# Kernel optimization log

Hardware: AMD Instinct MI355X
Metric: run time of the kernel (lower is better)

Reference implementation:

```python
import jax, jax.numpy as jnp
import numpy as np

V, E, H, G, L, T, B = 32000, 1024, 16, 4, 8, 1024, 2
NKV = H // G          # kv heads = 4
D = E // H            # head dim = 64
BLOCK = 1024          # block_size
EPS = 1e-5


def setup_inputs() -> dict:
    key = jax.random.key(0)
    ks = jax.random.split(key, 12)
    f32 = jnp.float32
    return {
        "idx": jax.random.randint(ks[0], (B, T), 0, V),
        "tok_emb": jax.random.normal(ks[1], (V, E), f32),
        "pos_emb": jax.random.normal(ks[2], (BLOCK, E), f32),
        "q_proj": jax.random.normal(ks[3], (L, E, G, NKV, D), f32) / E**0.5,
        "kv_proj": jax.random.normal(ks[4], (L, 2, E, NKV, D), f32) / E**0.5,
        "out_proj": jax.random.normal(ks[5], (L, E, E), f32) / (D * H)**0.5,
        "fc_in": jax.random.normal(ks[6], (L, E, 4 * E), f32) / E**0.5,
        "fc_out": jax.random.normal(ks[7], (L, 4 * E, E), f32) / (4 * E)**0.5,
        "scale": jnp.ones((L, 2, E), f32),
        "out_scale": jnp.ones((E,), f32),
        "lm_head": jax.random.normal(ks[8], (E, V), f32) / E**0.5,
    }


def _ln(x, w):
    mu = jnp.mean(x, axis=-1, keepdims=True)
    var = jnp.var(x, axis=-1, keepdims=True)
    return (x - mu) * jax.lax.rsqrt(var + EPS) * w


def reference(idx, tok_emb, pos_emb, q_proj, kv_proj, out_proj, fc_in, fc_out, scale, out_scale, lm_head):
    x = tok_emb[idx] + pos_emb[:T]                         # [B,T,E]
    causal = jnp.tril(jnp.ones((T, T), bool))              # [T,T]
    neg_inf = jnp.float32(-jnp.inf)

    def layer(x, params):
        w_kv, w_q, w_out, fc1, fc2, lscale = params
        h = _ln(x, lscale[0])                              # pre-LN (note: residual uses h, matching source)
        q = jnp.einsum('btc,cgnd->bgntd', h, w_q)          # [B,G,NKV,T,D]
        kv = jnp.einsum('btc,scnd->sbntd', h, w_kv)        # [2,B,NKV,T,D]
        k, v = kv[0], kv[1]
        att = jnp.einsum('bgnqd,bnkd->bgnqk', q, k) * (D ** -0.5)
        att = jnp.where(causal, att, neg_inf)
        att = jax.nn.softmax(att, axis=-1)
        o = jnp.einsum('bgnqk,bnkd->bgnqd', att, v)        # [B,G,NKV,T,D]
        o = jnp.transpose(o, (0, 3, 1, 2, 4)).reshape(B, T, E)
        o = jnp.einsum('btc,cd->btd', o, w_out)
        h = h + o
        h = _ln(h, lscale[1])
        mlp = jax.nn.relu(jnp.einsum('btc,cf->btf', h, fc1))
        mlp = jnp.einsum('btf,fc->btc', mlp, fc2)
        return h + mlp, None

    x, _ = jax.lax.scan(layer, x, (kv_proj, q_proj, out_proj, fc_in, fc_out, scale))
    x = _ln(x, out_scale)
    logits = jnp.einsum('btc,cv->btv', x, lm_head)         # [B,T,V]
    return logits
```

## Files before the change

kernel.cpp:

```cpp
#include <hip/hip_runtime.h>
#include <hip/hip_bf16.h>

typedef __attribute__((ext_vector_type(8))) short bf16x8;
typedef __attribute__((ext_vector_type(4))) short bf16x4;
typedef __attribute__((ext_vector_type(4))) float f32x4;

#define LB __launch_bounds__(256)

__device__ __forceinline__ unsigned short f2b(float f) {
  __hip_bfloat16 h = __float2bfloat16(f);
  return __builtin_bit_cast(unsigned short, h);
}

#define GLDS(gp, lp)                                                        \
  __builtin_amdgcn_global_load_lds(                                         \
      (const __attribute__((address_space(1))) void*)(gp),                  \
      (__attribute__((address_space(3))) void*)(lp), 16, 0, 0)

__global__ LB void embed_kernel(const int* __restrict__ idx, const float* __restrict__ tok,
                                const float* __restrict__ pos, float* __restrict__ X) {
  const int m = blockIdx.x;
  const int t = m & 1023;
  const int token = idx[m];
  const int c = threadIdx.x * 4;
  const float4 a = *(const float4*)(tok + (size_t)token * 1024 + c);
  const float4 p = *(const float4*)(pos + (size_t)t * 1024 + c);
  float4 o; o.x = a.x + p.x; o.y = a.y + p.y; o.z = a.z + p.z; o.w = a.w + p.w;
  *(float4*)(X + (size_t)m * 1024 + c) = o;
}

template<bool WF32>
__global__ LB void ln_kernel(const float* __restrict__ X, const float* __restrict__ W,
                             float* __restrict__ Yf, unsigned short* __restrict__ Yb) {
  const int row = blockIdx.x;
  const float* xr = X + (size_t)row * 1024;
  const int c = threadIdx.x * 4;
  const float4 v = *(const float4*)(xr + c);
  float s = v.x + v.y + v.z + v.w;
  float q = v.x*v.x + v.y*v.y + v.z*v.z + v.w*v.w;
  #pragma unroll
  for (int d = 32; d > 0; d >>= 1) { s += __shfl_down(s, d); q += __shfl_down(q, d); }
  __shared__ float ss[4], sq[4];
  const int wid = threadIdx.x >> 6;
  if ((threadIdx.x & 63) == 0) { ss[wid] = s; sq[wid] = q; }
  __syncthreads();
  const float fs = ss[0] + ss[1] + ss[2] + ss[3];
  const float fq = sq[0] + sq[1] + sq[2] + sq[3];
  const float mean = fs * (1.0f / 1024.0f);
  const float var = fq * (1.0f / 1024.0f) - mean * mean;
  const float rstd = rsqrtf(var + 1e-5f);
  const float4 w = *(const float4*)(W + c);
  float4 o;
  o.x = (v.x - mean) * rstd * w.x; o.y = (v.y - mean) * rstd * w.y;
  o.z = (v.z - mean) * rstd * w.z; o.w = (v.w - mean) * rstd * w.w;
  if (WF32) *(float4*)(Yf + (size_t)row * 1024 + c) = o;
  unsigned long long pk = (unsigned long long)f2b(o.x)
      | ((unsigned long long)f2b(o.y) << 16)
      | ((unsigned long long)f2b(o.z) << 32)
      | ((unsigned long long)f2b(o.w) << 48);
  *(unsigned long long*)(Yb + (size_t)row * 1024 + c) = pk;
}

__device__ __forceinline__ void tr_body(const float* __restrict__ src,
                                        unsigned short* __restrict__ dst,
                                        int C, int rowOff, int ldDst, int bx, int by) {
  __shared__ float tile[32][33];
  const int c0 = bx * 32, r0 = by * 32;
  const int tx = threadIdx.x & 31, ty = threadIdx.x >> 5;
  #pragma unroll
  for (int u = 0; u < 4; ++u)
    tile[ty + u * 8][tx] = src[(size_t)(r0 + ty + u * 8) * C + c0 + tx];
  __syncthreads();
  const int ci = threadIdx.x >> 4;
  const int rp = threadIdx.x & 15;
  #pragma unroll
  for (int u = 0; u < 2; ++u) {
    const int c = ci + u * 16;
    unsigned int pk = (unsigned int)f2b(tile[rp * 2][c])
                    | ((unsigned int)f2b(tile[rp * 2 + 1][c]) << 16);
    *(unsigned int*)&dst[(size_t)(rowOff + c0 + c) * ldDst + r0 + rp * 2] = pk;
  }
}

__global__ LB void transpose_w(const float* __restrict__ src, unsigned short* __restrict__ dst,
                               int C, int rowOff, int ldDst) {
  tr_body(src, dst, C, rowOff, ldDst, blockIdx.x, blockIdx.y);
}

__global__ LB void transpose_qkvo(const float* __restrict__ qp, const float* __restrict__ op,
                                  const float* __restrict__ kvp, unsigned short* __restrict__ dst) {
  int id = blockIdx.x;
  const float* src; int C, rowOff, bx, by;
  if (id < 2048) {
    src = (id < 1024) ? qp : op;
    rowOff = (id < 1024) ? 0 : 1536;
    id &= 1023; C = 1024; bx = id & 31; by = id >> 5;
  } else {
    id -= 2048;
    src = (id < 256) ? kvp : (kvp + 1024 * 256);
    rowOff = (id < 256) ? 1024 : 1280;
    id &= 255; C = 256; bx = id & 7; by = id >> 3;
  }
  tr_body(src, dst, C, rowOff, 1024, bx, by);
}

__global__ LB void transpose_fc(const float* __restrict__ f1, const float* __restrict__ f2,
                                unsigned short* __restrict__ F1T, unsigned short* __restrict__ F2T) {
  int id = blockIdx.x;
  if (id < 4096) {
    tr_body(f1, F1T, 4096, 0, 1024, id & 127, id >> 7);
  } else {
    id -= 4096;
    tr_body(f2, F2T, 1024, 0, 4096, id & 31, id >> 5);
  }
}

__global__ LB void transpose_v(const unsigned short* __restrict__ src, unsigned short* __restrict__ dst) {
  __shared__ unsigned short tile[32][33];
  const int b = blockIdx.z;
  const int c0 = blockIdx.x * 32, t0 = blockIdx.y * 32;
  const int tx = threadIdx.x & 31, ty = threadIdx.x >> 5;
  #pragma unroll
  for (int u = 0; u < 4; ++u)
    tile[ty + u * 8][tx] = src[(size_t)(b * 1024 + t0 + ty + u * 8) * 1536 + 1280 + c0 + tx];
  __syncthreads();
  #pragma unroll
  for (int u = 0; u < 4; ++u)
    dst[((size_t)b * 256 + c0 + ty + u * 8) * 1024 + t0 + tx] = tile[tx][ty + u * 8];
}

__global__ LB void attn_fused(const unsigned short* __restrict__ qkvb,
                              const unsigned short* __restrict__ vT,
                              unsigned short* __restrict__ ob) {
  const int qt = blockIdx.x, bh = blockIdx.y;
  const int b = bh >> 4, hh = bh & 15, n = hh & 3;
  const int tid = threadIdx.x, lane = tid & 63, w = tid >> 6;
  const int g = lane >> 4, c = lane & 15;
  const int q0w = qt * 128 + w * 32;
  const int kdiag = q0w >> 6;

  __shared__ unsigned short lsK[64 * 64];
  __shared__ unsigned short lsV[64 * 64];
  __shared__ unsigned short lsP[4][32 * 64];
  unsigned short* Pw = lsP[w];

  bf16x8 qf[2][2];
  {
    const unsigned short* Qb = qkvb + (size_t)(b * 1024 + q0w) * 1536 + hh * 64;
    #pragma unroll
    for (int nj = 0; nj < 2; ++nj)
      #pragma unroll
      for (int ks = 0; ks < 2; ++ks)
        qf[nj][ks] = *(const bf16x8*)(Qb + (size_t)(nj * 16 + c) * 1536 + ks * 32 + g * 8);
  }

  f32x4 accO[2][4] = {};
  float mrow[2] = {-1e30f, -1e30f};
  float lrow[2] = {0.0f, 0.0f};

  const int srow = tid >> 3;
  const int scol = ((tid & 7) ^ (srow & 7)) << 3;
  const unsigned short* gK = qkvb + (size_t)(b * 1024 + srow) * 1536 + 1024 + n * 64 + scol;
  const unsigned short* gV = vT + (size_t)((b * 4 + n) * 64 + srow) * 1024 + scol;
  unsigned short* lK = lsK + tid * 8;
  unsigned short* lV = lsV + tid * 8;

  const int ktmax = 2 * qt + 1;
  for (int kt = 0; kt <= ktmax; ++kt) {
    if (kt) __syncthreads();
    GLDS(gK + (size_t)kt * 64 * 1536, lK);
    GLDS(gK + (size_t)kt * 64 * 1536 + (size_t)32 * 1536, lK + 2048);
    GLDS(gV + (size_t)kt * 64, lV);
    GLDS(gV + (size_t)kt * 64 + (size_t)32 * 1024, lV + 2048);
    __syncthreads();
    if (kt > kdiag) continue;

    const bool dg = (kt == kdiag);
    const int kb = kt * 64;

    f32x4 st[4][2] = {};
    #pragma unroll
    for (int ks = 0; ks < 2; ++ks) {
      const int col = (((ks * 4 + g) ^ (lane & 7)) << 3);
      bf16x8 kf[4];
      #pragma unroll
      for (int mi = 0; mi < 4; ++mi)
        kf[mi] = *(const bf16x8*)&lsK[(mi * 16 + c) * 64 + col];
      #pragma unroll
      for (int mi = 0; mi < 4; ++mi)
        #pragma unroll
        for (int nj = 0; nj < 2; ++nj)
          st[mi][nj] = __builtin_amdgcn_mfma_f32_16x16x32_bf16(kf[mi], qf[nj][ks], st[mi][nj], 0, 0, 0);
    }

    float alv[2];
    #pragma unroll
    for (int nj = 0; nj < 2; ++nj) {
      const int qrow = q0w + nj * 16 + c;
      float mx = mrow[nj];
      #pragma unroll
      for (int mi = 0; mi < 4; ++mi)
        #pragma unroll
        for (int j = 0; j < 4; ++j) {
          float v = st[mi][nj][j] * 0.125f;
          if (dg && (kb + mi * 16 + g * 4 + j) > qrow) v = -1e30f;
          st[mi][nj][j] = v;
          mx = fmaxf(mx, v);
        }
      mx = fmaxf(mx, __shfl_xor(mx, 16));
      mx = fmaxf(mx, __shfl_xor(mx, 32));
      const float al = __expf(mrow[nj] - mx);
      float sum = 0.0f;
      #pragma unroll
      for (int mi = 0; mi < 4; ++mi) {
        bf16x4 pk;
        #pragma unroll
        for (int j = 0; j < 4; ++j) {
          const float e = __expf(st[mi][nj][j] - mx);
          sum += e;
          pk[j] = (short)f2b(e);
        }
        *(bf16x4*)&Pw[(nj * 16 + c) * 64 + ((mi * 16 + g * 4) ^ ((c & 7) << 3))] = pk;
      }
      sum += __shfl_xor(sum, 16);
      sum += __shfl_xor(sum, 32);
      lrow[nj] = lrow[nj] * al + sum;
      mrow[nj] = mx;
      alv[nj] = al;
    }

    #pragma unroll
    for (int mi = 0; mi < 2; ++mi) {
      float aj[4];
      #pragma unroll
      for (int j = 0; j < 4; ++j) aj[j] = __shfl(alv[mi], g * 4 + j);
      #pragma unroll
      for (int dj = 0; dj < 4; ++dj)
        #pragma unroll
        for (int j = 0; j < 4; ++j) accO[mi][dj][j] *= aj[j];
    }

    #pragma unroll
    for (int ks = 0; ks < 2; ++ks) {
      const int col = (((ks * 4 + g) ^ (lane & 7)) << 3);
      bf16x8 pa[2], vf[4];
      #pragma unroll
      for (int mi = 0; mi < 2; ++mi)
        pa[mi] = *(const bf16x8*)&Pw[(mi * 16 + c) * 64 + col];
      #pragma unroll
      for (int dj = 0; dj < 4; ++dj)
        vf[dj] = *(const bf16x8*)&lsV[(dj * 16 + c) * 64 + col];
      #pragma unroll
      for (int mi = 0; mi < 2; ++mi)
        #pragma unroll
        for (int dj = 0; dj < 4; ++dj)
          accO[mi][dj] = __builtin_amdgcn_mfma_f32_16x16x32_bf16(pa[mi], vf[dj], accO[mi][dj], 0, 0, 0);
    }
  }

  float linv[2] = {1.0f / lrow[0], 1.0f / lrow[1]};
  unsigned short* obase = ob + (size_t)(b * 1024 + q0w) * 1024 + hh * 64;
  #pragma unroll
  for (int mi = 0; mi < 2; ++mi) {
    float lj[4];
    #pragma unroll
    for (int j = 0; j < 4; ++j) lj[j] = __shfl(linv[mi], g * 4 + j);
    #pragma unroll
    for (int dj = 0; dj < 4; ++dj)
      #pragma unroll
      for (int j = 0; j < 4; ++j)
        obase[(size_t)(mi * 16 + g * 4 + j) * 1024 + dj * 16 + c] = f2b(accO[mi][dj][j] * lj[j]);
  }
}

template<int BM, int BN, bool BF16OUT, bool RELU, bool RESID>
__global__ LB void gemm_nt(const unsigned short* __restrict__ A, const unsigned short* __restrict__ Bt,
                           void* __restrict__ Cv, const float* __restrict__ Res,
                           int K, int lda, int ldb, int ldc) {
  constexpr int BK = 64;
  constexpr int WM = BM / 2, WN = BN / 2;
  constexpr int FM = WM / 16, FN = WN / 16;
  constexpr int PA = BM / 32, PB = BN / 32;
  int f = blockIdx.x + gridDim.x * blockIdx.y;
  const int nwg = gridDim.x * gridDim.y;
  if ((nwg & 7) == 0) f = (f & 7) * (nwg >> 3) + (f >> 3);
  const int bx = f % gridDim.x, by = f / gridDim.x;

  const int tid = threadIdx.x;
  const int lane = tid & 63, wid = tid >> 6;
  const int wr = wid >> 1, wc = wid & 1;
  const int m0 = bx * BM, n0 = by * BN;

  __shared__ unsigned short lsA[BM * BK];
  __shared__ unsigned short lsB[BN * BK];

  f32x4 acc[FM][FN] = {};

  const int srow = tid >> 3;
  const int scol = ((tid & 7) ^ (srow & 7)) << 3;
  const unsigned short* gA = A + (size_t)(m0 + srow) * lda + scol;
  const unsigned short* gB = Bt + (size_t)(n0 + srow) * ldb + scol;
  unsigned short* lA = lsA + tid * 8;
  unsigned short* lB = lsB + tid * 8;

  const int fr = lane & 15;
  const int j7 = lane & 7;
  const int g4 = lane >> 4;

  for (int k0 = 0; k0 < K; k0 += BK) {
    if (k0) __syncthreads();
    #pragma unroll
    for (int p = 0; p < PA; ++p)
      GLDS(gA + (size_t)(p * 32) * lda + k0, lA + p * 2048);
    #pragma unroll
    for (int p = 0; p < PB; ++p)
      GLDS(gB + (size_t)(p * 32) * ldb + k0, lB + p * 2048);
    __syncthreads();

    #pragma unroll
    for (int ks = 0; ks < 2; ++ks) {
      const int col = (((ks * 4 + g4) ^ j7) << 3);
      bf16x8 af[FM], bfv[FN];
      #pragma unroll
      for (int mi = 0; mi < FM; ++mi)
        af[mi] = *(const bf16x8*)&lsA[(wr * WM + mi * 16 + fr) * BK + col];
      #pragma unroll
      for (int nj = 0; nj < FN; ++nj)
        bfv[nj] = *(const bf16x8*)&lsB[(wc * WN + nj * 16 + fr) * BK + col];
      #pragma unroll
      for (int mi = 0; mi < FM; ++mi)
        #pragma unroll
        for (int nj = 0; nj < FN; ++nj)
          acc[mi][nj] = __builtin_amdgcn_mfma_f32_16x16x32_bf16(af[mi], bfv[nj], acc[mi][nj], 0, 0, 0);
    }
  }

  const int r0 = (lane >> 4) * 4, c0 = lane & 15;
  #pragma unroll
  for (int mi = 0; mi < FM; ++mi) {
    #pragma unroll
    for (int nj = 0; nj < FN; ++nj) {
      const int c = n0 + wc * WN + nj * 16 + c0;
      #pragma unroll
      for (int j = 0; j < 4; ++j) {
        const int r = m0 + wr * WM + mi * 16 + r0 + j;
        float v = acc[mi][nj][j];
        if (RELU) v = fmaxf(v, 0.0f);
        if (RESID) v += Res[(size_t)r * ldc + c];
        const size_t o = (size_t)r * ldc + c;
        if (BF16OUT) ((unsigned short*)Cv)[o] = f2b(v);
        else ((float*)Cv)[o] = v;
      }
    }
  }
}

extern "C" void kernel_launch(void* const* d_in, const int* in_sizes, int n_in,
                              void* d_out, int out_size, void* d_ws, size_t ws_size,
                              hipStream_t stream) {
  (void)in_sizes; (void)n_in; (void)out_size;
  const int*   idx      = (const int*)d_in[0];
  const float* tok_emb  = (const float*)d_in[1];
  const float* pos_emb  = (const float*)d_in[2];
  const float* q_proj   = (const float*)d_in[3];
  const float* kv_proj  = (const float*)d_in[4];
  const float* out_proj = (const float*)d_in[5];
  const float* fc_in    = (const float*)d_in[6];
  const float* fc_out   = (const float*)d_in[7];
  const float* scale    = (const float*)d_in[8];
  const float* out_scl  = (const float*)d_in[9];
  const float* lm_head  = (const float*)d_in[10];
  float* out = (float*)d_out;

  char* ws = (char*)d_ws;
  size_t off = 0;
  auto alloc = [&](size_t bytes) -> void* {
    void* p = ws + off;
    off += (bytes + 255) & ~(size_t)255;
    return p;
  };
  unsigned short* WqkvT = (unsigned short*)alloc((size_t)2560 * 1024 * 2);
  unsigned short* WoT   = WqkvT + (size_t)1536 * 1024;
  unsigned short* F1T   = (unsigned short*)alloc((size_t)4096 * 1024 * 2);
  unsigned short* F2T   = (unsigned short*)alloc((size_t)1024 * 4096 * 2);
  float*  xbuf  = (float*)alloc((size_t)2048 * 1024 * 4);
  float*  hbuf  = (float*)alloc((size_t)2048 * 1024 * 4);
  float*  h2buf = (float*)alloc((size_t)2048 * 1024 * 4);
  unsigned short* actb  = (unsigned short*)alloc((size_t)2048 * 1024 * 2);
  unsigned short* qkvb  = (unsigned short*)alloc((size_t)2048 * 1536 * 2);
  unsigned short* vT    = (unsigned short*)alloc((size_t)2 * 256 * 1024 * 2);
  unsigned short* LmT   = (unsigned short*)alloc((size_t)32000 * 1024 * 2);
  unsigned short* ob    = (unsigned short*)alloc((size_t)2048 * 1024 * 2);
  unsigned short* m1    = (unsigned short*)alloc((size_t)2048 * 4096 * 2);
  if (off > ws_size) return;

  const dim3 thr(256);

  embed_kernel<<<dim3(2048), thr, 0, stream>>>(idx, tok_emb, pos_emb, xbuf);

  for (int l = 0; l < 8; ++l) {
    const float* qp  = q_proj + (size_t)l * 1024 * 1024;
    const float* op  = out_proj + (size_t)l * 1024 * 1024;
    const float* kvp = kv_proj + (size_t)l * 2 * 1024 * 256;
    transpose_qkvo<<<dim3(2560), thr, 0, stream>>>(qp, op, kvp, WqkvT);
    transpose_fc<<<dim3(8192), thr, 0, stream>>>(
        fc_in + (size_t)l * 1024 * 4096, fc_out + (size_t)l * 4096 * 1024, F1T, F2T);

    const float* w1 = scale + (size_t)l * 2048;
    const float* w2 = w1 + 1024;

    ln_kernel<true><<<dim3(2048), thr, 0, stream>>>(xbuf, w1, hbuf, actb);
    gemm_nt<128, 64, true, false, false><<<dim3(16, 24), thr, 0, stream>>>(
        actb, WqkvT, qkvb, nullptr, 1024, 1024, 1024, 1536);
    transpose_v<<<dim3(8, 32, 2), thr, 0, stream>>>(qkvb, vT);
    attn_fused<<<dim3(8, 32), thr, 0, stream>>>(qkvb, vT, ob);
    gemm_nt<128, 64, false, false, true><<<dim3(16, 16), thr, 0, stream>>>(
        ob, WoT, xbuf, hbuf, 1024, 1024, 1024, 1024);
    ln_kernel<true><<<dim3(2048), thr, 0, stream>>>(xbuf, w2, h2buf, actb);
    gemm_nt<128, 128, true, true, false><<<dim3(16, 32), thr, 0, stream>>>(
        actb, F1T, m1, nullptr, 1024, 1024, 1024, 4096);
    gemm_nt<128, 64, false, false, true><<<dim3(16, 16), thr, 0, stream>>>(
        m1, F2T, xbuf, h2buf, 4096, 4096, 4096, 1024);
  }

  transpose_w<<<dim3(1000, 32), thr, 0, stream>>>(lm_head, LmT, 32000, 0, 1024);
  ln_kernel<false><<<dim3(2048), thr, 0, stream>>>(xbuf, out_scl, nullptr, actb);
  gemm_nt<128, 128, false, false, false><<<dim3(16, 250), thr, 0, stream>>>(
      actb, LmT, out, nullptr, 1024, 1024, 1024, 32000);
}
```

Baseline: 1.702 ms.

## Add 256x256 double-buffered GEMM kernel for the LM head projection

Adds a dedicated 512-thread GEMM with 256x256 output tiles, double-buffered LDS filled by direct global-to-LDS loads, an XOR-swizzled LDS layout, and an XCD-aware block remapping. The final vocab projection now uses it instead of the generic 128x128 kernel. The goal is to raise arithmetic intensity and overlap loads with MFMA work on the largest GEMM. In exchange it uses 128 KB of LDS and a large accumulator array, which limits occupancy and may cause register spills.

```diff
diff --git a/kernel.cpp b/kernel.cpp
--- a/kernel.cpp
+++ b/kernel.cpp
@@ -350,6 +350,100 @@
         const size_t o = (size_t)r * ldc + c;
         if (BF16OUT) ((unsigned short*)Cv)[o] = f2b(v);
         else ((float*)Cv)[o] = v;
+      }
+    }
+  }
+}
+
+__global__ __launch_bounds__(512) void gemm_big(const unsigned short* __restrict__ A,
+                                                const unsigned short* __restrict__ Bt,
+                                                float* __restrict__ C,
+                                                int K, int lda, int ldb, int ldc) {
+  int f = blockIdx.x + gridDim.x * blockIdx.y;
+  const int nwg = gridDim.x * gridDim.y;
+  f = (f & 7) * (nwg >> 3) + (f >> 3);
+  const int bx = f % gridDim.x, by = f / gridDim.x;
+  const int m0 = bx * 256, n0 = by * 256;
+
+  const int tid = threadIdx.x;
+  const int lane = tid & 63, wid = tid >> 6;
+  const int wr = wid >> 2, wc = wid & 3;
+  const int fr = lane & 15, g4 = lane >> 4, j7 = lane & 7;
+
+  __shared__ unsigned short lsA[2][256 * 64];
+  __shared__ unsigned short lsB[2][256 * 64];
+
+  f32x4 acc[8][4] = {};
+
+  const int srow = tid >> 3;
+  const int scol = ((tid & 7) ^ (srow & 7)) << 3;
+  const unsigned short* gA = A + (size_t)(m0 + srow) * lda + scol;
+  const unsigned short* gB = Bt + (size_t)(n0 + srow) * ldb + scol;
+
+  const int nt = K >> 6;
+
+  {
+    unsigned short* pA = &lsA[0][tid * 8];
+    unsigned short* pB = &lsB[0][tid * 8];
+    #pragma unroll
+    for (int p = 0; p < 4; ++p) GLDS(gA + (size_t)(p * 64) * lda, pA + p * 4096);
+    #pragma unroll
+    for (int p = 0; p < 4; ++p) GLDS(gB + (size_t)(p * 64) * ldb, pB + p * 4096);
+  }
+  __syncthreads();
+
+  for (int t = 0; t < nt; ++t) {
+    const int bi = t & 1;
+    const bool pref = (t + 1) < nt;
+    const int k1 = (t + 1) << 6;
+    unsigned short* pA = &lsA[bi ^ 1][tid * 8];
+    unsigned short* pB = &lsB[bi ^ 1][tid * 8];
+    const unsigned short* TA = lsA[bi];
+    const unsigned short* TB = lsB[bi];
+
+    #pragma unroll
+    for (int q = 0; q < 4; ++q) {
+      const int qm = q & 1, qn = q >> 1;
+      bf16x8 af[2][4], bf[2][2];
+      #pragma unroll
+      for (int ks = 0; ks < 2; ++ks) {
+        const int col = (((ks * 4 + g4) ^ j7) << 3);
+        #pragma unroll
+        for (int mi = 0; mi < 4; ++mi)
+          af[ks][mi] = *(const bf16x8*)&TA[(wr * 128 + (qm * 4 + mi) * 16 + fr) * 64 + col];
+        #pragma unroll
+        for (int nj = 0; nj < 2; ++nj)
+          bf[ks][nj] = *(const bf16x8*)&TB[(wc * 64 + (qn * 2 + nj) * 16 + fr) * 64 + col];
+      }
+      if (pref) {
+        GLDS(gA + (size_t)(q * 64) * lda + k1, pA + q * 4096);
+        GLDS(gB + (size_t)(q * 64) * ldb + k1, pB + q * 4096);
+      }
+      __builtin_amdgcn_s_barrier();
+      __builtin_amdgcn_s_setprio(1);
+      #pragma unroll
+      for (int ks = 0; ks < 2; ++ks)
+        #pragma unroll
+        for (int mi = 0; mi < 4; ++mi)
+          #pragma unroll
+          for (int nj = 0; nj < 2; ++nj)
+            acc[qm * 4 + mi][qn * 2 + nj] = __builtin_amdgcn_mfma_f32_16x16x32_bf16(
+                af[ks][mi], bf[ks][nj], acc[qm * 4 + mi][qn * 2 + nj], 0, 0, 0);
+      __builtin_amdgcn_s_setprio(0);
+      __builtin_amdgcn_s_barrier();
+    }
+    __syncthreads();
+  }
+
+  #pragma unroll
+  for (int mi = 0; mi < 8; ++mi) {
+    #pragma unroll
+    for (int nj = 0; nj < 4; ++nj) {
+      const int cc = n0 + wc * 64 + nj * 16 + fr;
+      #pragma unroll
+      for (int j = 0; j < 4; ++j) {
+        const int rr = m0 + wr * 128 + mi * 16 + g4 * 4 + j;
+        C[(size_t)rr * ldc + cc] = acc[mi][nj][j];
       }
     }
   }
@@ -425,6 +519,5 @@
 
   transpose_w<<<dim3(1000, 32), thr, 0, stream>>>(lm_head, LmT, 32000, 0, 1024);
   ln_kernel<false><<<dim3(2048), thr, 0, stream>>>(xbuf, out_scl, nullptr, actb);
-  gemm_nt<128, 128, false, false, false><<<dim3(16, 250), thr, 0, stream>>>(
-      actb, LmT, out, nullptr, 1024, 1024, 1024, 32000);
-}
+  gemm_big<<<dim3(8, 125), dim3(512), 0, stream>>>(actb, LmT, out, 1024, 1024, 1024, 32000);
+}
```

Measured after the change: 1.713 ms. No clear change (+0.6%).

## Retile attention to 64-row query blocks with double-buffered K/V and reversed scheduling

Applied to the files above, without the earlier changes.

The attention kernel now gives each block 64 query rows instead of 128, with 16 rows per wave, which doubles the grid to 512 blocks. K/V tiles are double-buffered so the next tile's global-to-LDS load is issued while the current tile is computed. The block index is reversed so the longest causal blocks start first, and key tiles past the diagonal are no longer loaded. The trade-off is less Q reuse per K/V tile load and more total K/V traffic, in exchange for better occupancy, load balance and overlap.

```diff
diff --git a/kernel.cpp b/kernel.cpp
--- a/kernel.cpp
+++ b/kernel.cpp
@@ -132,145 +132,130 @@
 __global__ LB void attn_fused(const unsigned short* __restrict__ qkvb,
                               const unsigned short* __restrict__ vT,
                               unsigned short* __restrict__ ob) {
-  const int qt = blockIdx.x, bh = blockIdx.y;
+  const int qt = 15 - blockIdx.x, bh = blockIdx.y;
   const int b = bh >> 4, hh = bh & 15, n = hh & 3;
   const int tid = threadIdx.x, lane = tid & 63, w = tid >> 6;
   const int g = lane >> 4, c = lane & 15;
-  const int q0w = qt * 128 + w * 32;
-  const int kdiag = q0w >> 6;
-
-  __shared__ unsigned short lsK[64 * 64];
-  __shared__ unsigned short lsV[64 * 64];
-  __shared__ unsigned short lsP[4][32 * 64];
+  const int q0w = qt * 64 + w * 16;
+  const int qrow = q0w + c;
+
+  __shared__ unsigned short lsK[2][64 * 64];
+  __shared__ unsigned short lsV[2][64 * 64];
+  __shared__ unsigned short lsP[4][16 * 64];
   unsigned short* Pw = lsP[w];
 
-  bf16x8 qf[2][2];
+  bf16x8 qf[2];
   {
     const unsigned short* Qb = qkvb + (size_t)(b * 1024 + q0w) * 1536 + hh * 64;
     #pragma unroll
-    for (int nj = 0; nj < 2; ++nj)
-      #pragma unroll
-      for (int ks = 0; ks < 2; ++ks)
-        qf[nj][ks] = *(const bf16x8*)(Qb + (size_t)(nj * 16 + c) * 1536 + ks * 32 + g * 8);
-  }
-
-  f32x4 accO[2][4] = {};
-  float mrow[2] = {-1e30f, -1e30f};
-  float lrow[2] = {0.0f, 0.0f};
+    for (int ks = 0; ks < 2; ++ks)
+      qf[ks] = *(const bf16x8*)(Qb + (size_t)c * 1536 + ks * 32 + g * 8);
+  }
+
+  f32x4 accO[4] = {};
+  float mr = -1e30f, lr = 0.0f;
 
   const int srow = tid >> 3;
   const int scol = ((tid & 7) ^ (srow & 7)) << 3;
   const unsigned short* gK = qkvb + (size_t)(b * 1024 + srow) * 1536 + 1024 + n * 64 + scol;
   const unsigned short* gV = vT + (size_t)((b * 4 + n) * 64 + srow) * 1024 + scol;
-  unsigned short* lK = lsK + tid * 8;
-  unsigned short* lV = lsV + tid * 8;
-
-  const int ktmax = 2 * qt + 1;
-  for (int kt = 0; kt <= ktmax; ++kt) {
-    if (kt) __syncthreads();
-    GLDS(gK + (size_t)kt * 64 * 1536, lK);
-    GLDS(gK + (size_t)kt * 64 * 1536 + (size_t)32 * 1536, lK + 2048);
-    GLDS(gV + (size_t)kt * 64, lV);
-    GLDS(gV + (size_t)kt * 64 + (size_t)32 * 1024, lV + 2048);
-    __syncthreads();
-    if (kt > kdiag) continue;
-
-    const bool dg = (kt == kdiag);
+
+  GLDS(gK, &lsK[0][tid * 8]);
+  GLDS(gK + (size_t)32 * 1536, &lsK[0][tid * 8 + 2048]);
+  GLDS(gV, &lsV[0][tid * 8]);
+  GLDS(gV + (size_t)32 * 1024, &lsV[0][tid * 8 + 2048]);
+  __syncthreads();
+
+  for (int kt = 0; kt <= qt; ++kt) {
+    const int cur = kt & 1;
+    if (kt < qt) {
+      const size_t ko = (size_t)(kt + 1) * 64;
+      GLDS(gK + ko * 1536, &lsK[cur ^ 1][tid * 8]);
+      GLDS(gK + (ko + 32) * 1536, &lsK[cur ^ 1][tid * 8 + 2048]);
+      GLDS(gV + ko, &lsV[cur ^ 1][tid * 8]);
+      GLDS(gV + ko + (size_t)32 * 1024, &lsV[cur ^ 1][tid * 8 + 2048]);
+    }
+    const unsigned short* K_ = lsK[cur];
+    const unsigned short* V_ = lsV[cur];
+    const bool dg = (kt == qt);
     const int kb = kt * 64;
 
-    f32x4 st[4][2] = {};
+    f32x4 st[4] = {};
     #pragma unroll
     for (int ks = 0; ks < 2; ++ks) {
       const int col = (((ks * 4 + g) ^ (lane & 7)) << 3);
       bf16x8 kf[4];
       #pragma unroll
       for (int mi = 0; mi < 4; ++mi)
-        kf[mi] = *(const bf16x8*)&lsK[(mi * 16 + c) * 64 + col];
+        kf[mi] = *(const bf16x8*)&K_[(mi * 16 + c) * 64 + col];
       #pragma unroll
       for (int mi = 0; mi < 4; ++mi)
-        #pragma unroll
-        for (int nj = 0; nj < 2; ++nj)
-          st[mi][nj] = __builtin_amdgcn_mfma_f32_16x16x32_bf16(kf[mi], qf[nj][ks], st[mi][nj], 0, 0, 0);
-    }
-
-    float alv[2];
-    #pragma unroll
-    for (int nj = 0; nj < 2; ++nj) {
-      const int qrow = q0w + nj * 16 + c;
-      float mx = mrow[nj];
-      #pragma unroll
-      for (int mi = 0; mi < 4; ++mi)
-        #pragma unroll
-        for (int j = 0; j < 4; ++j) {
-          float v = st[mi][nj][j] * 0.125f;
-          if (dg && (kb + mi * 16 + g * 4 + j) > qrow) v = -1e30f;
-          st[mi][nj][j] = v;
-          mx = fmaxf(mx, v);
-        }
-      mx = fmaxf(mx, __shfl_xor(mx, 16));
-      mx = fmaxf(mx, __shfl_xor(mx, 32));
-      const float al = __expf(mrow[nj] - mx);
-      float sum = 0.0f;
-      #pragma unroll
-      for (int mi = 0; mi < 4; ++mi) {
-        bf16x4 pk;
-        #pragma unroll
-        for (int j = 0; j < 4; ++j) {
-          const float e = __expf(st[mi][nj][j] - mx);
-          sum += e;
-          pk[j] = (short)f2b(e);
-        }
-        *(bf16x4*)&Pw[(nj * 16 + c) * 64 + ((mi * 16 + g * 4) ^ ((c & 7) << 3))] = pk;
+        st[mi] = __builtin_amdgcn_mfma_f32_16x16x32_bf16(kf[mi], qf[ks], st[mi], 0, 0, 0);
+    }
+
+    float mx = mr;
+    #pragma unroll
+    for (int mi = 0; mi < 4; ++mi)
+      #pragma unroll
+      for (int j = 0; j < 4; ++j) {
+        float v = st[mi][j] * 0.125f;
+        if (dg && (kb + mi * 16 + g * 4 + j) > qrow) v = -1e30f;
+        st[mi][j] = v;
+        mx = fmaxf(mx, v);
       }
-      sum += __shfl_xor(sum, 16);
-      sum += __shfl_xor(sum, 32);
-      lrow[nj] = lrow[nj] * al + sum;
-      mrow[nj] = mx;
-      alv[nj] = al;
-    }
-
-    #pragma unroll
-    for (int mi = 0; mi < 2; ++mi) {
-      float aj[4];
-      #pragma unroll
-      for (int j = 0; j < 4; ++j) aj[j] = __shfl(alv[mi], g * 4 + j);
+    mx = fmaxf(mx, __shfl_xor(mx, 16));
+    mx = fmaxf(mx, __shfl_xor(mx, 32));
+    const float al = __expf(mr - mx);
+    float sum = 0.0f;
+    #pragma unroll
+    for (int mi = 0; mi < 4; ++mi) {
+      bf16x4 pk;
+      #pragma unroll
+      for (int j = 0; j < 4; ++j) {
+        const float e = __expf(st[mi][j] - mx);
+        sum += e;
+        pk[j] = (short)f2b(e);
+      }
+      *(bf16x4*)&Pw[c * 64 + ((mi * 16 + g * 4) ^ ((c & 7) << 3))] = pk;
+    }
+    sum += __shfl_xor(sum, 16);
+    sum += __shfl_xor(sum, 32);
+    lr = lr * al + sum;
+    mr = mx;
+
+    float aj[4];
+    #pragma unroll
+    for (int j = 0; j < 4; ++j) aj[j] = __shfl(al, g * 4 + j);
+    #pragma unroll
+    for (int dj = 0; dj < 4; ++dj)
+      #pragma unroll
+      for (int j = 0; j < 4; ++j) accO[dj][j] *= aj[j];
+
+    #pragma unroll
+    for (int ks = 0; ks < 2; ++ks) {
+      const int col = (((ks * 4 + g) ^ (c & 7)) << 3);
+      const bf16x8 pa = *(const bf16x8*)&Pw[c * 64 + col];
+      bf16x8 vf[4];
       #pragma unroll
       for (int dj = 0; dj < 4; ++dj)
-        #pragma unroll
-        for (int j = 0; j < 4; ++j) accO[mi][dj][j] *= aj[j];
-    }
-
-    #pragma unroll
-    for (int ks = 0; ks < 2; ++ks) {
-      const int col = (((ks * 4 + g) ^ (lane & 7)) << 3);
-      bf16x8 pa[2], vf[4];
-      #pragma unroll
-      for (int mi = 0; mi < 2; ++mi)
-        pa[mi] = *(const bf16x8*)&Pw[(mi * 16 + c) * 64 + col];
+        vf[dj] = *(const bf16x8*)&V_[(dj * 16 + c) * 64 + col];
       #pragma unroll
       for (int dj = 0; dj < 4; ++dj)
-        vf[dj] = *(const bf16x8*)&lsV[(dj * 16 + c) * 64 + col];
-      #pragma unroll
-      for (int mi = 0; mi < 2; ++mi)
-        #pragma unroll
-        for (int dj = 0; dj < 4; ++dj)
-          accO[mi][dj] = __builtin_amdgcn_mfma_f32_16x16x32_bf16(pa[mi], vf[dj], accO[mi][dj], 0, 0, 0);
-    }
-  }
-
-  float linv[2] = {1.0f / lrow[0], 1.0f / lrow[1]};
+        accO[dj] = __builtin_amdgcn_mfma_f32_16x16x32_bf16(pa, vf[dj], accO[dj], 0, 0, 0);
+    }
+    __syncthreads();
+  }
+
+  const float linv = 1.0f / lr;
+  float lj[4];
+  #pragma unroll
+  for (int j = 0; j < 4; ++j) lj[j] = __shfl(linv, g * 4 + j);
   unsigned short* obase = ob + (size_t)(b * 1024 + q0w) * 1024 + hh * 64;
   #pragma unroll
-  for (int mi = 0; mi < 2; ++mi) {
-    float lj[4];
-    #pragma unroll
-    for (int j = 0; j < 4; ++j) lj[j] = __shfl(linv[mi], g * 4 + j);
-    #pragma unroll
-    for (int dj = 0; dj < 4; ++dj)
-      #pragma unroll
-      for (int j = 0; j < 4; ++j)
-        obase[(size_t)(mi * 16 + g * 4 + j) * 1024 + dj * 16 + c] = f2b(accO[mi][dj][j] * lj[j]);
-  }
+  for (int dj = 0; dj < 4; ++dj)
+    #pragma unroll
+    for (int j = 0; j < 4; ++j)
+      obase[(size_t)(g * 4 + j) * 1024 + dj * 16 + c] = f2b(accO[dj][j] * lj[j]);
 }
 
 template<int BM, int BN, bool BF16OUT, bool RELU, bool RESID>
@@ -413,7 +398,7 @@
     gemm_nt<128, 64, true, false, false><<<dim3(16, 24), thr, 0, stream>>>(
         actb, WqkvT, qkvb, nullptr, 1024, 1024, 1024, 1536);
     transpose_v<<<dim3(8, 32, 2), thr, 0, stream>>>(qkvb, vT);
-    attn_fused<<<dim3(8, 32), thr, 0, stream>>>(qkvb, vT, ob);
+    attn_fused<<<dim3(16, 32), thr, 0, stream>>>(qkvb, vT, ob);
     gemm_nt<128, 64, false, false, true><<<dim3(16, 16), thr, 0, stream>>>(
         ob, WoT, xbuf, hbuf, 1024, 1024, 1024, 1024);
     ln_kernel<true><<<dim3(2048), thr, 0, stream>>>(xbuf, w2, h2buf, actb);
```

Measured after the change: 1.625 ms. -4.5%, faster.
